# Optimization experiments

Measured on AMD Instinct MI355X. Metric: run time of the kernel, lower is better.

The kernel has to match this reference:

```python
import jax, jax.numpy as jnp
import numpy as np

FORGET_BIAS = 1.0

def _lstm_layer(x_seq, W, b):
    # x_seq: [T, B, D]; W: [D+H, 4H]; b: [4H]
    T, B, _ = x_seq.shape
    H = W.shape[1] // 4
    def step(carry, x):
        c, h = carry
        z = jnp.concatenate([x, h], axis=1) @ W + b  # [B, 4H]
        i, j, f, o = jnp.split(z, 4, axis=1)          # BasicLSTMCell gate order
        new_c = c * jax.nn.sigmoid(f + FORGET_BIAS) + jax.nn.sigmoid(i) * jnp.tanh(j)
        new_h = jnp.tanh(new_c) * jax.nn.sigmoid(o)
        return (new_c, new_h), new_h
    init = (jnp.zeros((B, H), x_seq.dtype), jnp.zeros((B, H), x_seq.dtype))
    _, out = jax.lax.scan(step, init, x_seq)
    return out  # [T, B, H]

def setup_inputs() -> dict:
    key = jax.random.key(0)
    k0, k1, k2 = jax.random.split(key, 3)
    T, B, D, H = 256, 64, 1024, 1024
    scale = 0.05  # keep gates out of saturation
    return {
        "input_seq": jax.random.normal(k0, (T, B, D), dtype=jnp.float32),
        "W0": jax.random.normal(k1, (D + H, 4 * H), dtype=jnp.float32) * scale,
        "b0": jnp.zeros((4 * H,), dtype=jnp.float32),
        "W1": jax.random.normal(k2, (H + H, 4 * H), dtype=jnp.float32) * scale,
        "b1": jnp.zeros((4 * H,), dtype=jnp.float32),
    }

def reference(input_seq, W0, b0, W1, b1):
    # 2-layer static LSTM (training=False -> no dropout)
    h1 = _lstm_layer(input_seq, W0, b0)
    h2 = _lstm_layer(h1, W1, b1)
    return h2
```

## Files before the change

### kernel.cpp

```cpp
#include <hip/hip_runtime.h>
#include <cmath>


typedef _Float16 half8 __attribute__((ext_vector_type(8)));
typedef float f32x4 __attribute__((ext_vector_type(4)));

constexpr int Tt = 256, Bb = 64, Kd = 1024, Gg = 4096;
constexpr int KT = 32;
constexpr size_t MT_ELEMS = (size_t)KT * 64 * 8;

__device__ __forceinline__ f32x4 zero4() { f32x4 z = {0.f, 0.f, 0.f, 0.f}; return z; }
__device__ __forceinline__ float sigmoidf_(float x) { return 1.f / (1.f + expf(-x)); }

__global__ void pack_w_kernel(const float* __restrict__ W0, const float* __restrict__ W1,
                              _Float16* __restrict__ WP0x, _Float16* __restrict__ WP0h,
                              _Float16* __restrict__ WP1x, _Float16* __restrict__ WP1h) {
    int idx = blockIdx.x * 256 + threadIdx.x;
    int half_id = blockIdx.y;
    const float* src = (half_id < 2) ? W0 : W1;
    int rowoff = (half_id & 1) * 1024;
    _Float16* dst = (half_id == 0) ? WP0x : (half_id == 1) ? WP0h : (half_id == 2) ? WP1x : WP1h;

    int lane = idx & 63;
    int kt = (idx >> 6) & 31;
    int nt = idx >> 11;
    int p = nt * 16 + (lane & 15);
    int col = (p & 3) * 1024 + (p >> 2);
    int kbase = rowoff + kt * 32 + (lane >> 4) * 8;
    half8 v;
#pragma unroll
    for (int j = 0; j < 8; ++j) v[j] = (_Float16)src[(size_t)(kbase + j) * Gg + col];
    *reinterpret_cast<half8*>(dst + (size_t)idx * 8) = v;
    (void)kt;
}

__global__ void pack_bias_kernel(const float* __restrict__ b0, const float* __restrict__ b1,
                                 float* __restrict__ bp0, float* __restrict__ bp1) {
    int idx = blockIdx.x * 256 + threadIdx.x;
    int l = idx >> 12, p = idx & 4095;
    int col = (p & 3) * 1024 + (p >> 2);
    (l ? bp1 : bp0)[p] = (l ? b1 : b0)[col];
}

__global__ void pack_a_kernel(const float* __restrict__ X, _Float16* __restrict__ XP) {
    int idx = blockIdx.x * 256 + threadIdx.x;
    int lane = idx & 63;
    int kt = (idx >> 6) & 31;
    int mt = idx >> 11;
    int m = mt * 16 + (lane & 15);
    int kbase = kt * 32 + (lane >> 4) * 8;
    const float* srow = X + (size_t)m * Kd + kbase;
    half8 v;
#pragma unroll
    for (int j = 0; j < 8; ++j) v[j] = (_Float16)srow[j];
    *reinterpret_cast<half8*>(XP + (size_t)idx * 8) = v;
}

__global__ __launch_bounds__(256) void xgemm_kernel(const _Float16* __restrict__ AP,
                                                    const _Float16* __restrict__ WP,
                                                    const float* __restrict__ bias,
                                                    float* __restrict__ Z) {
    int lane = threadIdx.x & 63, wave = threadIdx.x >> 6;
    int wrow = wave >> 1, wcol = wave & 1;
    int mtb = blockIdx.x * 8 + wrow * 4;
    int ntb = blockIdx.y * 8 + wcol * 4;

    f32x4 acc[4][4];
#pragma unroll
    for (int i = 0; i < 4; ++i)
#pragma unroll
        for (int j = 0; j < 4; ++j) acc[i][j] = zero4();

    for (int kt = 0; kt < KT; ++kt) {
        half8 a[4], b[4];
#pragma unroll
        for (int i = 0; i < 4; ++i)
            a[i] = *reinterpret_cast<const half8*>(AP + (((size_t)(mtb + i) * KT + kt) * 64 + lane) * 8);
#pragma unroll
        for (int j = 0; j < 4; ++j)
            b[j] = *reinterpret_cast<const half8*>(WP + (((size_t)(ntb + j) * KT + kt) * 64 + lane) * 8);
#pragma unroll
        for (int i = 0; i < 4; ++i)
#pragma unroll
            for (int j = 0; j < 4; ++j)
                acc[i][j] = __builtin_amdgcn_mfma_f32_16x16x32_f16(a[i], b[j], acc[i][j], 0, 0, 0);
    }

    int r0 = (lane >> 4) * 4, cc = lane & 15;
#pragma unroll
    for (int j = 0; j < 4; ++j) {
        int p = (ntb + j) * 16 + cc;
        float bs = bias[p];
#pragma unroll
        for (int i = 0; i < 4; ++i) {
            int mbase = (mtb + i) * 16 + r0;
#pragma unroll
            for (int r = 0; r < 4; ++r)
                Z[(size_t)(mbase + r) * Gg + p] = acc[i][j][r] + bs;
        }
    }
}

__global__ __launch_bounds__(256) void lstm_step_kernel(const float* __restrict__ ZT,
                                                        const _Float16* __restrict__ hprev,
                                                        const _Float16* __restrict__ WPh,
                                                        float* __restrict__ c,
                                                        _Float16* __restrict__ houtA,
                                                        float* __restrict__ houtF) {
    int lane = threadIdx.x & 63, w = threadIdx.x >> 6;
    int nt = blockIdx.x;

    f32x4 acc = zero4();
    for (int kt = 0; kt < KT; ++kt) {
        half8 a = *reinterpret_cast<const half8*>(hprev + (((size_t)w * KT + kt) * 64 + lane) * 8);
        half8 b = *reinterpret_cast<const half8*>(WPh + (((size_t)nt * KT + kt) * 64 + lane) * 8);
        acc = __builtin_amdgcn_mfma_f32_16x16x32_f16(a, b, acc, 0, 0, 0);
    }

    __shared__ float zs[4][16][17];
    int q = lane >> 4, cc = lane & 15;
#pragma unroll
    for (int r = 0; r < 4; ++r)
        zs[w][q * 4 + r][cc] = acc[r] + ZT[(size_t)(w * 16 + q * 4 + r) * Gg + nt * 16 + cc];
    __syncthreads();

    int bl = lane >> 2, hl = lane & 3;
    float zi = zs[w][bl][hl * 4 + 0];
    float zj = zs[w][bl][hl * 4 + 1];
    float zf = zs[w][bl][hl * 4 + 2];
    float zo = zs[w][bl][hl * 4 + 3];
    int b = w * 16 + bl;
    int hcol = nt * 4 + hl;
    float cold = c[(size_t)b * 1024 + hcol];
    float cn = cold * sigmoidf_(zf + 1.0f) + sigmoidf_(zi) * tanhf(zj);
    float hn = tanhf(cn) * sigmoidf_(zo);
    c[(size_t)b * 1024 + hcol] = cn;
    houtA[(((size_t)w * KT + (hcol >> 5)) * 64 + ((hcol >> 3) & 3) * 16 + bl) * 8 + (hcol & 7)] = (_Float16)hn;
    if (houtF) houtF[(size_t)b * 1024 + hcol] = hn;
}

extern "C" void kernel_launch(void* const* d_in, const int* in_sizes, int n_in,
                              void* d_out, int out_size, void* d_ws, size_t ws_size,
                              hipStream_t stream) {
    const float* X  = (const float*)d_in[0];
    const float* W0 = (const float*)d_in[1];
    const float* b0 = (const float*)d_in[2];
    const float* W1 = (const float*)d_in[3];
    const float* b1 = (const float*)d_in[4];
    float* out = (float*)d_out;

    char* ws = (char*)d_ws;
    size_t off = 0;
    auto take = [&](size_t n) -> void* {
        void* r = ws + off;
        off += (n + 255) & ~(size_t)255;
        return r;
    };

    const size_t WPB = (size_t)Kd * Gg * 2;
    _Float16* WP0x = (_Float16*)take(WPB);
    _Float16* WP0h = (_Float16*)take(WPB);
    _Float16* WP1x = (_Float16*)take(WPB);
    _Float16* WP1h = (_Float16*)take(WPB);
    float* bp0 = (float*)take(Gg * 4);
    float* bp1 = (float*)take(Gg * 4);
    const size_t APB = (size_t)Tt * Bb * Kd * 2;
    _Float16* XP  = (_Float16*)take(APB);
    _Float16* H1P = (_Float16*)take(APB);
    _Float16* hzero = (_Float16*)take((size_t)Bb * 1024 * 2);
    _Float16* h2A   = (_Float16*)take((size_t)2 * Bb * 1024 * 2);
    float* c0 = (float*)take((size_t)Bb * 1024 * 4);
    float* c1 = (float*)take((size_t)Bb * 1024 * 4);

    int Tc = 256;
    while (Tc > 8 && off + (size_t)Tc * Bb * Gg * 4 > ws_size) Tc >>= 1;
    float* Z = (float*)take((size_t)Tc * Bb * Gg * 4);

    hipMemsetAsync(hzero, 0, (size_t)Bb * 1024 * 2, stream);
    hipMemsetAsync(h2A, 0, (size_t)2 * Bb * 1024 * 2, stream);
    hipMemsetAsync(c0, 0, (size_t)Bb * 1024 * 4, stream);
    hipMemsetAsync(c1, 0, (size_t)Bb * 1024 * 4, stream);

    pack_w_kernel<<<dim3(2048, 4), 256, 0, stream>>>(W0, W1, WP0x, WP0h, WP1x, WP1h);
    pack_bias_kernel<<<32, 256, 0, stream>>>(b0, b1, bp0, bp1);
    pack_a_kernel<<<8192, 256, 0, stream>>>(X, XP);

    const size_t hstep = 4 * MT_ELEMS;

    for (int t0 = 0; t0 < Tt; t0 += Tc) {
        xgemm_kernel<<<dim3(Tc * Bb / 128, Gg / 128), 256, 0, stream>>>(
            XP + (size_t)t0 * hstep / 16 * 16, WP0x, bp0, Z);
        for (int t = t0; t < t0 + Tc; ++t) {
            const _Float16* hp = (t == 0) ? hzero : H1P + (size_t)(t - 1) * hstep;
            lstm_step_kernel<<<256, 256, 0, stream>>>(
                Z + (size_t)(t - t0) * Bb * Gg, hp, WP0h, c0,
                H1P + (size_t)t * hstep, nullptr);
        }
    }
    for (int t0 = 0; t0 < Tt; t0 += Tc) {
        xgemm_kernel<<<dim3(Tc * Bb / 128, Gg / 128), 256, 0, stream>>>(
            H1P + (size_t)t0 * hstep, WP1x, bp1, Z);
        for (int t = t0; t < t0 + Tc; ++t) {
            const _Float16* hp = h2A + (size_t)(t & 1) * Bb * 1024;
            _Float16* hw = h2A + (size_t)((t + 1) & 1) * Bb * 1024;
            lstm_step_kernel<<<256, 256, 0, stream>>>(
                Z + (size_t)(t - t0) * Bb * Gg, hp, WP1h, c1,
                hw, out + (size_t)t * Bb * 1024);
        }
    }
    (void)in_sizes; (void)n_in; (void)out_size;
}
```

Before: 3.364 ms.

## Fuse both LSTM layers into one persistent cooperative kernel with LDS-resident weights

Replaces the per-timestep kernel launches and the separate input-projection GEMM with a single persistent kernel of 256 blocks. Each block keeps its 32-column slice of the combined [x,h] weight matrix in LDS, computes the gates for each timestep, and holds the cell state in registers. Layer 1 runs one timestep behind layer 0 as a wavefront, and a software grid barrier separates the steps. This removes about 512 launch overheads and the large Z buffer round trip. In exchange it depends on all blocks being co-resident, uses a spin-barrier with a timeout, and reduces partial sums with LDS atomics.

```diff
diff --git a/kernel.cpp b/kernel.cpp
--- a/kernel.cpp
+++ b/kernel.cpp
@@ -5,33 +5,30 @@
 typedef _Float16 half8 __attribute__((ext_vector_type(8)));
 typedef float f32x4 __attribute__((ext_vector_type(4)));
 
-constexpr int Tt = 256, Bb = 64, Kd = 1024, Gg = 4096;
-constexpr int KT = 32;
-constexpr size_t MT_ELEMS = (size_t)KT * 64 * 8;
-
-__device__ __forceinline__ f32x4 zero4() { f32x4 z = {0.f, 0.f, 0.f, 0.f}; return z; }
+constexpr int Tt = 256, Gg = 4096;
+constexpr size_t HPACK = 65536;
+constexpr int NBLK = 256;
+constexpr unsigned WLDS_BYTES = 131072;
+constexpr unsigned ZP_FLOATS = 8 * 16 * 17;
+constexpr unsigned SMEM_BYTES = WLDS_BYTES + ZP_FLOATS * 4;
+
 __device__ __forceinline__ float sigmoidf_(float x) { return 1.f / (1.f + expf(-x)); }
 
 __global__ void pack_w_kernel(const float* __restrict__ W0, const float* __restrict__ W1,
-                              _Float16* __restrict__ WP0x, _Float16* __restrict__ WP0h,
-                              _Float16* __restrict__ WP1x, _Float16* __restrict__ WP1h) {
+                              _Float16* __restrict__ WP0, _Float16* __restrict__ WP1) {
     int idx = blockIdx.x * 256 + threadIdx.x;
-    int half_id = blockIdx.y;
-    const float* src = (half_id < 2) ? W0 : W1;
-    int rowoff = (half_id & 1) * 1024;
-    _Float16* dst = (half_id == 0) ? WP0x : (half_id == 1) ? WP0h : (half_id == 2) ? WP1x : WP1h;
-
+    const float* src = blockIdx.y ? W1 : W0;
+    _Float16* dst = blockIdx.y ? WP1 : WP0;
     int lane = idx & 63;
-    int kt = (idx >> 6) & 31;
-    int nt = idx >> 11;
+    int kt = (idx >> 6) & 63;
+    int nt = idx >> 12;
     int p = nt * 16 + (lane & 15);
     int col = (p & 3) * 1024 + (p >> 2);
-    int kbase = rowoff + kt * 32 + (lane >> 4) * 8;
+    int kbase = kt * 32 + (lane >> 4) * 8;
     half8 v;
 #pragma unroll
     for (int j = 0; j < 8; ++j) v[j] = (_Float16)src[(size_t)(kbase + j) * Gg + col];
     *reinterpret_cast<half8*>(dst + (size_t)idx * 8) = v;
-    (void)kt;
 }
 
 __global__ void pack_bias_kernel(const float* __restrict__ b0, const float* __restrict__ b1,
@@ -49,94 +46,123 @@
     int mt = idx >> 11;
     int m = mt * 16 + (lane & 15);
     int kbase = kt * 32 + (lane >> 4) * 8;
-    const float* srow = X + (size_t)m * Kd + kbase;
+    const float* srow = X + (size_t)m * 1024 + kbase;
     half8 v;
 #pragma unroll
     for (int j = 0; j < 8; ++j) v[j] = (_Float16)srow[j];
     *reinterpret_cast<half8*>(XP + (size_t)idx * 8) = v;
 }
 
-__global__ __launch_bounds__(256) void xgemm_kernel(const _Float16* __restrict__ AP,
-                                                    const _Float16* __restrict__ WP,
-                                                    const float* __restrict__ bias,
-                                                    float* __restrict__ Z) {
-    int lane = threadIdx.x & 63, wave = threadIdx.x >> 6;
-    int wrow = wave >> 1, wcol = wave & 1;
-    int mtb = blockIdx.x * 8 + wrow * 4;
-    int ntb = blockIdx.y * 8 + wcol * 4;
-
-    f32x4 acc[4][4];
-#pragma unroll
-    for (int i = 0; i < 4; ++i)
-#pragma unroll
-        for (int j = 0; j < 4; ++j) acc[i][j] = zero4();
-
-    for (int kt = 0; kt < KT; ++kt) {
-        half8 a[4], b[4];
-#pragma unroll
-        for (int i = 0; i < 4; ++i)
-            a[i] = *reinterpret_cast<const half8*>(AP + (((size_t)(mtb + i) * KT + kt) * 64 + lane) * 8);
-#pragma unroll
-        for (int j = 0; j < 4; ++j)
-            b[j] = *reinterpret_cast<const half8*>(WP + (((size_t)(ntb + j) * KT + kt) * 64 + lane) * 8);
-#pragma unroll
-        for (int i = 0; i < 4; ++i)
-#pragma unroll
-            for (int j = 0; j < 4; ++j)
-                acc[i][j] = __builtin_amdgcn_mfma_f32_16x16x32_f16(a[i], b[j], acc[i][j], 0, 0, 0);
-    }
-
-    int r0 = (lane >> 4) * 4, cc = lane & 15;
-#pragma unroll
-    for (int j = 0; j < 4; ++j) {
-        int p = (ntb + j) * 16 + cc;
-        float bs = bias[p];
-#pragma unroll
-        for (int i = 0; i < 4; ++i) {
-            int mbase = (mtb + i) * 16 + r0;
-#pragma unroll
-            for (int r = 0; r < 4; ++r)
-                Z[(size_t)(mbase + r) * Gg + p] = acc[i][j][r] + bs;
+__device__ __forceinline__ void grid_barrier(unsigned* cnt, unsigned* gen) {
+    __syncthreads();
+    if (threadIdx.x == 0) {
+        unsigned g = __hip_atomic_load(gen, __ATOMIC_RELAXED, __HIP_MEMORY_SCOPE_AGENT);
+        unsigned arr = __hip_atomic_fetch_add(cnt, 1u, __ATOMIC_ACQ_REL, __HIP_MEMORY_SCOPE_AGENT);
+        if (arr == NBLK - 1) {
+            __hip_atomic_store(cnt, 0u, __ATOMIC_RELAXED, __HIP_MEMORY_SCOPE_AGENT);
+            __hip_atomic_store(gen, g + 1u, __ATOMIC_RELEASE, __HIP_MEMORY_SCOPE_AGENT);
+        } else {
+            unsigned spins = 0;
+            while (__hip_atomic_load(gen, __ATOMIC_RELAXED, __HIP_MEMORY_SCOPE_AGENT) == g) {
+                __builtin_amdgcn_s_sleep(2);
+                if (++spins > (1u << 24)) break;
+            }
+            __builtin_amdgcn_fence(__ATOMIC_ACQUIRE, "agent");
         }
     }
-}
-
-__global__ __launch_bounds__(256) void lstm_step_kernel(const float* __restrict__ ZT,
-                                                        const _Float16* __restrict__ hprev,
-                                                        const _Float16* __restrict__ WPh,
-                                                        float* __restrict__ c,
-                                                        _Float16* __restrict__ houtA,
-                                                        float* __restrict__ houtF) {
-    int lane = threadIdx.x & 63, w = threadIdx.x >> 6;
-    int nt = blockIdx.x;
-
-    f32x4 acc = zero4();
-    for (int kt = 0; kt < KT; ++kt) {
-        half8 a = *reinterpret_cast<const half8*>(hprev + (((size_t)w * KT + kt) * 64 + lane) * 8);
-        half8 b = *reinterpret_cast<const half8*>(WPh + (((size_t)nt * KT + kt) * 64 + lane) * 8);
-        acc = __builtin_amdgcn_mfma_f32_16x16x32_f16(a, b, acc, 0, 0, 0);
-    }
-
-    __shared__ float zs[4][16][17];
-    int q = lane >> 4, cc = lane & 15;
-#pragma unroll
-    for (int r = 0; r < 4; ++r)
-        zs[w][q * 4 + r][cc] = acc[r] + ZT[(size_t)(w * 16 + q * 4 + r) * Gg + nt * 16 + cc];
     __syncthreads();
-
-    int bl = lane >> 2, hl = lane & 3;
-    float zi = zs[w][bl][hl * 4 + 0];
-    float zj = zs[w][bl][hl * 4 + 1];
-    float zf = zs[w][bl][hl * 4 + 2];
-    float zo = zs[w][bl][hl * 4 + 3];
-    int b = w * 16 + bl;
-    int hcol = nt * 4 + hl;
-    float cold = c[(size_t)b * 1024 + hcol];
-    float cn = cold * sigmoidf_(zf + 1.0f) + sigmoidf_(zi) * tanhf(zj);
-    float hn = tanhf(cn) * sigmoidf_(zo);
-    c[(size_t)b * 1024 + hcol] = cn;
-    houtA[(((size_t)w * KT + (hcol >> 5)) * 64 + ((hcol >> 3) & 3) * 16 + bl) * 8 + (hcol & 7)] = (_Float16)hn;
-    if (houtF) houtF[(size_t)b * 1024 + hcol] = hn;
+}
+
+struct FArgs {
+    const _Float16* XP;
+    const _Float16* WP0;
+    const _Float16* WP1;
+    const float* bp0;
+    const float* bp1;
+    _Float16* h1p;
+    _Float16* h2p;
+    float* out;
+    unsigned* bar;
+};
+
+__global__ __launch_bounds__(1024, 4) void lstm_fused(FArgs a) {
+    extern __shared__ char smem[];
+    _Float16* wlds = (_Float16*)smem;
+    float* zp = (float*)(smem + WLDS_BYTES);
+
+    const int tid = threadIdx.x;
+    const int layer = blockIdx.x >> 7;
+    const int cg = blockIdx.x & 127;
+
+    const _Float16* wsrc = (layer ? a.WP1 : a.WP0) + (size_t)cg * 65536;
+    for (int i = tid; i < 8192; i += 1024)
+        ((half8*)wlds)[i] = ((const half8*)wsrc)[i];
+    for (int i = tid; i < (int)ZP_FLOATS; i += 1024) zp[i] = 0.f;
+
+    float creg = 0.f;
+    float bias4[4] = {0.f, 0.f, 0.f, 0.f};
+    if (tid < 512) {
+        int hl = tid & 7;
+        const float* bp = layer ? a.bp1 : a.bp0;
+#pragma unroll
+        for (int g = 0; g < 4; ++g) bias4[g] = bp[cg * 32 + hl * 4 + g];
+    }
+    __syncthreads();
+
+    const int lane = tid & 63, wv = tid >> 6;
+    const int mt = wv & 3, kq = wv >> 2;
+    const int r0 = (lane >> 4) * 4, ccc = lane & 15;
+    const int ktL = (kq & 1) * 16;
+
+    for (int s = 0; s <= Tt; ++s) {
+        const bool act = layer ? (s >= 1) : (s < Tt);
+        if (act) {
+            const _Float16* h1prev = a.h1p + (size_t)((s + 1) & 1) * HPACK;
+            const _Float16* srcA;
+            if (layer == 0)
+                srcA = (kq < 2) ? (a.XP + (size_t)s * HPACK) : h1prev;
+            else
+                srcA = (kq < 2) ? h1prev : (a.h2p + (size_t)(s & 1) * HPACK);
+
+            const half8* ap = (const half8*)srcA + ((size_t)mt * 32 + ktL) * 64 + lane;
+            const half8* bq0 = (const half8*)wlds + ((size_t)(0 * 64 + kq * 16)) * 64 + lane;
+            const half8* bq1 = (const half8*)wlds + ((size_t)(1 * 64 + kq * 16)) * 64 + lane;
+            f32x4 ac0 = {0.f, 0.f, 0.f, 0.f}, ac1 = {0.f, 0.f, 0.f, 0.f};
+#pragma unroll
+            for (int i = 0; i < 16; ++i) {
+                half8 av = ap[i * 64];
+                ac0 = __builtin_amdgcn_mfma_f32_16x16x32_f16(av, bq0[i * 64], ac0, 0, 0, 0);
+                ac1 = __builtin_amdgcn_mfma_f32_16x16x32_f16(av, bq1[i * 64], ac1, 0, 0, 0);
+            }
+#pragma unroll
+            for (int r = 0; r < 4; ++r) {
+                atomicAdd(&zp[((mt * 2 + 0) * 16 + r0 + r) * 17 + ccc], ac0[r]);
+                atomicAdd(&zp[((mt * 2 + 1) * 16 + r0 + r) * 17 + ccc], ac1[r]);
+            }
+        }
+        __syncthreads();
+        if (act && tid < 512) {
+            int b = tid >> 3, hl = tid & 7;
+            float z[4];
+#pragma unroll
+            for (int g = 0; g < 4; ++g) {
+                int c = hl * 4 + g;
+                z[g] = zp[(((b >> 4) * 2 + (c >> 4)) * 16 + (b & 15)) * 17 + (c & 15)] + bias4[g];
+            }
+            float cn = creg * sigmoidf_(z[2] + 1.0f) + sigmoidf_(z[0]) * tanhf(z[1]);
+            float hn = tanhf(cn) * sigmoidf_(z[3]);
+            creg = cn;
+            int k = cg * 8 + hl;
+            _Float16* hdst = layer ? (a.h2p + (size_t)((s + 1) & 1) * HPACK)
+                                   : (a.h1p + (size_t)(s & 1) * HPACK);
+            hdst[(((size_t)(b >> 4) * 32 + (k >> 5)) * 64 + ((k >> 3) & 3) * 16 + (b & 15)) * 8 + (k & 7)] =
+                (_Float16)hn;
+            if (layer) a.out[(size_t)(s - 1) * 65536 + (size_t)b * 1024 + k] = hn;
+        }
+        __syncthreads();
+        for (int i = tid; i < (int)ZP_FLOATS; i += 1024) zp[i] = 0.f;
+        grid_barrier(a.bar, a.bar + 1);
+    }
 }
 
 extern "C" void kernel_launch(void* const* d_in, const int* in_sizes, int n_in,
@@ -157,56 +183,34 @@
         return r;
     };
 
-    const size_t WPB = (size_t)Kd * Gg * 2;
-    _Float16* WP0x = (_Float16*)take(WPB);
-    _Float16* WP0h = (_Float16*)take(WPB);
-    _Float16* WP1x = (_Float16*)take(WPB);
-    _Float16* WP1h = (_Float16*)take(WPB);
+    const size_t WPB = (size_t)2048 * Gg * 2;
+    _Float16* WP0 = (_Float16*)take(WPB);
+    _Float16* WP1 = (_Float16*)take(WPB);
     float* bp0 = (float*)take(Gg * 4);
     float* bp1 = (float*)take(Gg * 4);
-    const size_t APB = (size_t)Tt * Bb * Kd * 2;
-    _Float16* XP  = (_Float16*)take(APB);
-    _Float16* H1P = (_Float16*)take(APB);
-    _Float16* hzero = (_Float16*)take((size_t)Bb * 1024 * 2);
-    _Float16* h2A   = (_Float16*)take((size_t)2 * Bb * 1024 * 2);
-    float* c0 = (float*)take((size_t)Bb * 1024 * 4);
-    float* c1 = (float*)take((size_t)Bb * 1024 * 4);
-
-    int Tc = 256;
-    while (Tc > 8 && off + (size_t)Tc * Bb * Gg * 4 > ws_size) Tc >>= 1;
-    float* Z = (float*)take((size_t)Tc * Bb * Gg * 4);
-
-    hipMemsetAsync(hzero, 0, (size_t)Bb * 1024 * 2, stream);
-    hipMemsetAsync(h2A, 0, (size_t)2 * Bb * 1024 * 2, stream);
-    hipMemsetAsync(c0, 0, (size_t)Bb * 1024 * 4, stream);
-    hipMemsetAsync(c1, 0, (size_t)Bb * 1024 * 4, stream);
-
-    pack_w_kernel<<<dim3(2048, 4), 256, 0, stream>>>(W0, W1, WP0x, WP0h, WP1x, WP1h);
+    const size_t APB = (size_t)Tt * 64 * 1024 * 2;
+    _Float16* XP = (_Float16*)take(APB);
+    _Float16* h1p = (_Float16*)take(2 * HPACK * 2);
+    _Float16* h2p = (_Float16*)take(2 * HPACK * 2);
+    unsigned* bar = (unsigned*)take(256);
+
+    hipMemsetAsync(h1p, 0, 2 * HPACK * 2, stream);
+    hipMemsetAsync(h2p, 0, 2 * HPACK * 2, stream);
+    hipMemsetAsync(bar, 0, 256, stream);
+
+    pack_w_kernel<<<dim3(4096, 2), 256, 0, stream>>>(W0, W1, WP0, WP1);
     pack_bias_kernel<<<32, 256, 0, stream>>>(b0, b1, bp0, bp1);
     pack_a_kernel<<<8192, 256, 0, stream>>>(X, XP);
 
-    const size_t hstep = 4 * MT_ELEMS;
-
-    for (int t0 = 0; t0 < Tt; t0 += Tc) {
-        xgemm_kernel<<<dim3(Tc * Bb / 128, Gg / 128), 256, 0, stream>>>(
-            XP + (size_t)t0 * hstep / 16 * 16, WP0x, bp0, Z);
-        for (int t = t0; t < t0 + Tc; ++t) {
-            const _Float16* hp = (t == 0) ? hzero : H1P + (size_t)(t - 1) * hstep;
-            lstm_step_kernel<<<256, 256, 0, stream>>>(
-                Z + (size_t)(t - t0) * Bb * Gg, hp, WP0h, c0,
-                H1P + (size_t)t * hstep, nullptr);
-        }
-    }
-    for (int t0 = 0; t0 < Tt; t0 += Tc) {
-        xgemm_kernel<<<dim3(Tc * Bb / 128, Gg / 128), 256, 0, stream>>>(
-            H1P + (size_t)t0 * hstep, WP1x, bp1, Z);
-        for (int t = t0; t < t0 + Tc; ++t) {
-            const _Float16* hp = h2A + (size_t)(t & 1) * Bb * 1024;
-            _Float16* hw = h2A + (size_t)((t + 1) & 1) * Bb * 1024;
-            lstm_step_kernel<<<256, 256, 0, stream>>>(
-                Z + (size_t)(t - t0) * Bb * Gg, hp, WP1h, c1,
-                hw, out + (size_t)t * Bb * 1024);
-        }
-    }
-    (void)in_sizes; (void)n_in; (void)out_size;
-}
+    hipFuncSetAttribute((const void*)lstm_fused,
+                        hipFuncAttributeMaxDynamicSharedMemorySize, SMEM_BYTES);
+
+    FArgs fa{XP, WP0, WP1, bp0, bp1, h1p, h2p, out, bar};
+    void* kp[] = {&fa};
+    hipError_t e = hipLaunchCooperativeKernel((const void*)lstm_fused, dim3(NBLK), dim3(1024),
+                                              kp, SMEM_BYTES, stream);
+    if (e != hipSuccess) {
+        lstm_fused<<<dim3(NBLK), dim3(1024), SMEM_BYTES, stream>>>(fa);
+    }
+    (void)in_sizes; (void)n_in; (void)out_size; (void)ws_size;
+}
```

After: 6.864 ms. 2.04x slower.
